# Kernel tuning notes

Hardware: AMD Instinct MI355X
Metric: run time of the kernel (lower is better)

## Reference

```python
import jax, jax.numpy as jnp
import numpy as np

N = 256           # rotation dimension (rows of X)
B = 8192          # columns / batch of vectors being rotated
N_THETAS = N * (N - 1) // 2


def _schedule(n):
    """Round-robin (circle method) tournament schedule.

    Returns pa, pb, tix each of shape [n-1, n//2]:
      round r applies disjoint Givens rotations to row pairs (pa[r,k], pb[r,k])
      using theta index tix[r,k] (lexicographic index of pair (i,j), i<j).
    """
    arr = list(range(n))
    pa, pb, tix = [], [], []
    for _ in range(n - 1):
        ra, rb, rt = [], [], []
        for k in range(n // 2):
            i, j = arr[k], arr[n - 1 - k]
            if i > j:
                i, j = j, i
            ra.append(i)
            rb.append(j)
            rt.append(i * n - i * (i + 1) // 2 + (j - i - 1))
        pa.append(ra)
        pb.append(rb)
        tix.append(rt)
        arr = [arr[0], arr[-1]] + arr[1:-1]
    return np.array(pa), np.array(pb), np.array(tix)


def setup_inputs() -> dict:
    key = jax.random.key(0)
    k1, k2 = jax.random.split(key)
    X = jax.random.normal(k1, (N, B), dtype=jnp.float32)
    thetas = jax.random.normal(k2, (N_THETAS,), dtype=jnp.float32) * 0.1
    return {"X": X, "thetas": thetas}


def reference(X, thetas):
    n = X.shape[0]
    pa_np, pb_np, tix_np = _schedule(n)          # static numpy, traced-time constants
    th = thetas[jnp.asarray(tix_np)]             # [n-1, n//2]
    c, s = jnp.cos(th), jnp.sin(th)
    pa = jnp.asarray(pa_np)
    pb = jnp.asarray(pb_np)

    def step(Xc, inp):
        a, b, cr, sr = inp                        # a,b: [n//2] row indices (disjoint)
        ra, rb = Xc[a], Xc[b]                     # [n//2, B]
        Xc = Xc.at[a].set(cr[:, None] * ra - sr[:, None] * rb)
        Xc = Xc.at[b].set(sr[:, None] * ra + cr[:, None] * rb)
        return Xc, None

    Xo, _ = jax.lax.scan(step, X, (pa, pb, c, s))  # n-1 sequential rounds
    return Xo
```

## Files before the change

kernel.cpp:

```cpp
#include <hip/hip_runtime.h>

#define NROT 256
#define NB   8192
#define TBL_ROUNDS 264

typedef _Float16 f16;
typedef _Float16 f16x8 __attribute__((ext_vector_type(8)));
typedef float    f32x4 __attribute__((ext_vector_type(4)));


__global__ void k_prep(const float* __restrict__ thetas, float4* __restrict__ tbl) {
    int idx = blockIdx.x * 256 + threadIdx.x;
    if (idx >= TBL_ROUNDS * 128) return;
    int r = idx >> 7;
    int k = idx & 127;
    if (r >= 255) {
        tbl[idx] = make_float4(1.0f, 0.0f, __int_as_float(0 | (1 << 16)), 0.0f);
        return;
    }
    int i, j;
    if (k == 0) {
        i = 0;
        j = (254 - r) + 1;
    } else {
        int m1 = k - 1 - r;   if (m1 < 0) m1 += 255;
        int m2 = 254 - k - r; if (m2 < 0) m2 += 255;
        int v1 = m1 + 1, v2 = m2 + 1;
        i = v1 < v2 ? v1 : v2;
        j = v1 < v2 ? v2 : v1;
    }
    int tix = i * 256 - (i * (i + 1)) / 2 + (j - i - 1);
    float th = thetas[tix];
    float s, c;
    sincosf(th, &s, &c);
    tbl[idx] = make_float4(c, s, __int_as_float(i | (j << 16)), 0.0f);
}

template <int ROFF>
__device__ __forceinline__ void rot_rounds64(const float4* __restrict__ t0, float* buf) {
    float4 e0[4], e1[4];
#pragma unroll
    for (int d = 0; d < 4; ++d) {
        e0[d] = t0[(ROFF + d) * 128];
        e1[d] = t0[(ROFF + d) * 128 + 1];
    }
#pragma unroll 4
    for (int it = 0; it < 64; ++it) {
        const int slot = it % 4;
        float4 E0 = e0[slot], E1 = e1[slot];
        e0[slot] = t0[(ROFF + it + 4) * 128];
        e1[slot] = t0[(ROFF + it + 4) * 128 + 1];

        int ij0 = __float_as_int(E0.z);
        int a0 = ij0 & 0xffff, b0 = ij0 >> 16;
        int ij1 = __float_as_int(E1.z);
        int a1 = ij1 & 0xffff, b1 = ij1 >> 16;

        float ra0 = buf[a0], rb0 = buf[b0];
        float ra1 = buf[a1], rb1 = buf[b1];
        float na0 = E0.x * ra0 - E0.y * rb0;
        float nb0 = E0.y * ra0 + E0.x * rb0;
        float na1 = E1.x * ra1 - E1.y * rb1;
        float nb1 = E1.y * ra1 + E1.x * rb1;
        buf[a0] = na0; buf[b0] = nb0;
        buf[a1] = na1; buf[b1] = nb1;
    }
}

__global__ __launch_bounds__(64) void k_rot(const float4* __restrict__ tbl,
                                            float* __restrict__ Rg) {
    __shared__ float buf[256];
    int l   = threadIdx.x;
    int grp = blockIdx.y;
    int c   = blockIdx.x;
#pragma unroll
    for (int q = 0; q < 4; ++q) {
        int m = l * 4 + q;
        buf[m] = (m == c) ? 1.0f : 0.0f;
    }
    const float4* t0 = tbl + 2 * l;
    if      (grp == 0) rot_rounds64<0>(t0, buf);
    else if (grp == 1) rot_rounds64<64>(t0, buf);
    else if (grp == 2) rot_rounds64<128>(t0, buf);
    else               rot_rounds64<192>(t0, buf);

    float* Rout = Rg + grp * (256 * 256);
#pragma unroll
    for (int q = 0; q < 4; ++q) {
        int m = l * 4 + q;
        Rout[m * 256 + c] = buf[m];
    }
}

__global__ __launch_bounds__(256) void k_merge4(const float* __restrict__ Rg,
                                                f16* __restrict__ Rh) {
    __shared__ float vcur[256];
    __shared__ float pacc[4][256];
    int t = threadIdx.x;
    int w = t >> 6;
    int l = t & 63;
    int r0 = blockIdx.x;

    if (t < 64)
        *(float4*)&vcur[t * 4] =
            *(const float4*)(Rg + 3 * 65536 + r0 * 256 + t * 4);
    __syncthreads();

    for (int g = 2; g >= 0; --g) {
        const float* A = Rg + g * 65536;
        int kbase = w * 64;
        float4 acc = make_float4(0.f, 0.f, 0.f, 0.f);
#pragma unroll 8
        for (int kk = 0; kk < 64; ++kk) {
            float  s = vcur[kbase + kk];
            float4 a = *(const float4*)(A + (kbase + kk) * 256 + l * 4);
            acc.x += s * a.x; acc.y += s * a.y;
            acc.z += s * a.z; acc.w += s * a.w;
        }
        *(float4*)&pacc[w][l * 4] = acc;
        __syncthreads();
        if (t < 64) {
            float4 p0 = *(float4*)&pacc[0][t * 4];
            float4 p1 = *(float4*)&pacc[1][t * 4];
            float4 p2 = *(float4*)&pacc[2][t * 4];
            float4 p3 = *(float4*)&pacc[3][t * 4];
            float4 sum = make_float4(p0.x + p1.x + p2.x + p3.x,
                                     p0.y + p1.y + p2.y + p3.y,
                                     p0.z + p1.z + p2.z + p3.z,
                                     p0.w + p1.w + p2.w + p3.w);
            if (g > 0) *(float4*)&vcur[t * 4] = sum;
            else {
                int o = r0 * 256 + t * 4;
                Rh[o + 0] = (f16)sum.x;
                Rh[o + 1] = (f16)sum.y;
                Rh[o + 2] = (f16)sum.z;
                Rh[o + 3] = (f16)sum.w;
            }
        }
        __syncthreads();
    }
}

__global__ __launch_bounds__(512) void k_gemm(const f16* __restrict__ Rh,
                                              const float* __restrict__ X,
                                              float* __restrict__ out) {
    __shared__ float Xf[256][32];
    __shared__ __align__(16) f16 Xh[32 * 256];
    int t  = threadIdx.x;
    int w  = t >> 6;
    int l  = t & 63;
    int n0 = blockIdx.x * 32;

#pragma unroll
    for (int p = 0; p < 4; ++p) {
        int idx = t + 512 * p;
        int n4  = idx & 7;
        int k   = idx >> 3;
        *(float4*)&Xf[k][n4 * 4] =
            *(const float4*)(X + (size_t)k * NB + n0 + n4 * 4);
    }
    __syncthreads();

    {
        int n  = t & 31;
        int k0 = (t >> 5) * 16;
        f16x8 h0, h1;
#pragma unroll
        for (int u = 0; u < 8; ++u) h0[u] = (f16)Xf[k0 + u][n];
#pragma unroll
        for (int u = 0; u < 8; ++u) h1[u] = (f16)Xf[k0 + 8 + u][n];
        int xv = (n & 7) * 8;
        *(f16x8*)&Xh[n * 256 + ((k0    ) ^ xv)] = h0;
        *(f16x8*)&Xh[n * 256 + ((k0 + 8) ^ xv)] = h1;
    }
    __syncthreads();

    f32x4 acc[2][2];
#pragma unroll
    for (int r = 0; r < 2; ++r)
#pragma unroll
        for (int c = 0; c < 2; ++c) acc[r][c] = (f32x4){0.f, 0.f, 0.f, 0.f};

    int lm = l & 15;
    int g  = l >> 4;
    int xv = (lm & 7) * 8;
#pragma unroll
    for (int s = 0; s < 8; ++s) {
        int koff = s * 32 + 8 * g;
        f16x8 a0 = *(const f16x8*)(Rh + (32 * w + lm) * 256 + koff);
        f16x8 a1 = *(const f16x8*)(Rh + (32 * w + 16 + lm) * 256 + koff);
        f16x8 b0 = *(const f16x8*)&Xh[lm * 256        + (koff ^ xv)];
        f16x8 b1 = *(const f16x8*)&Xh[(16 + lm) * 256 + (koff ^ xv)];
        acc[0][0] = __builtin_amdgcn_mfma_f32_16x16x32_f16(a0, b0, acc[0][0], 0, 0, 0);
        acc[0][1] = __builtin_amdgcn_mfma_f32_16x16x32_f16(a0, b1, acc[0][1], 0, 0, 0);
        acc[1][0] = __builtin_amdgcn_mfma_f32_16x16x32_f16(a1, b0, acc[1][0], 0, 0, 0);
        acc[1][1] = __builtin_amdgcn_mfma_f32_16x16x32_f16(a1, b1, acc[1][1], 0, 0, 0);
    }

#pragma unroll
    for (int r = 0; r < 2; ++r)
#pragma unroll
        for (int c = 0; c < 2; ++c)
#pragma unroll
            for (int q = 0; q < 4; ++q)
                out[(size_t)(32 * w + 16 * r + 4 * g + q) * NB + n0 + 16 * c + lm] =
                    acc[r][c][q];
}

extern "C" void kernel_launch(void* const* d_in, const int* in_sizes, int n_in,
                              void* d_out, int out_size, void* d_ws, size_t ws_size,
                              hipStream_t stream) {
    const float* X      = (const float*)d_in[0];
    const float* thetas = (const float*)d_in[1];
    float* out = (float*)d_out;
    char*  ws  = (char*)d_ws;

    float4* tbl = (float4*)ws;
    float*  Rg  = (float*)(ws + 540672);
    f16*    Rh  = (f16*)(ws + 1589248);

    k_prep  <<<dim3(132),    dim3(256), 0, stream>>>(thetas, tbl);
    k_rot   <<<dim3(256, 4), dim3(64),  0, stream>>>(tbl, Rg);
    k_merge4<<<dim3(256),    dim3(256), 0, stream>>>(Rg, Rh);
    k_gemm  <<<dim3(256),    dim3(512), 0, stream>>>(Rh, X, out);
}
```

Before: 39.42 us.

## Keep rotation state in registers with wave shuffles and tree-merge partial products

```diff
diff --git a/kernel.cpp b/kernel.cpp
--- a/kernel.cpp
+++ b/kernel.cpp
@@ -5,140 +5,144 @@
 #define TBL_ROUNDS 264
 
 typedef _Float16 f16;
+typedef _Float16 f16x4 __attribute__((ext_vector_type(4)));
 typedef _Float16 f16x8 __attribute__((ext_vector_type(8)));
 typedef float    f32x4 __attribute__((ext_vector_type(4)));
 
 
-__global__ void k_prep(const float* __restrict__ thetas, float4* __restrict__ tbl) {
+__global__ void k_prep(const float* __restrict__ thetas, float2* __restrict__ cs) {
     int idx = blockIdx.x * 256 + threadIdx.x;
     if (idx >= TBL_ROUNDS * 128) return;
     int r = idx >> 7;
     int k = idx & 127;
-    if (r >= 255) {
-        tbl[idx] = make_float4(1.0f, 0.0f, __int_as_float(0 | (1 << 16)), 0.0f);
-        return;
-    }
+    if (r >= 255) { cs[idx] = make_float2(1.0f, 0.0f); return; }
     int i, j;
+    bool swapped = false;
     if (k == 0) {
         i = 0;
-        j = (254 - r) + 1;
+        j = 255 - r;
     } else {
         int m1 = k - 1 - r;   if (m1 < 0) m1 += 255;
         int m2 = 254 - k - r; if (m2 < 0) m2 += 255;
         int v1 = m1 + 1, v2 = m2 + 1;
-        i = v1 < v2 ? v1 : v2;
-        j = v1 < v2 ? v2 : v1;
+        swapped = v1 > v2;
+        i = swapped ? v2 : v1;
+        j = swapped ? v1 : v2;
     }
     int tix = i * 256 - (i * (i + 1)) / 2 + (j - i - 1);
     float th = thetas[tix];
     float s, c;
     sincosf(th, &s, &c);
-    tbl[idx] = make_float4(c, s, __int_as_float(i | (j << 16)), 0.0f);
-}
-
-template <int ROFF>
-__device__ __forceinline__ void rot_rounds64(const float4* __restrict__ t0, float* buf) {
-    float4 e0[4], e1[4];
-#pragma unroll
-    for (int d = 0; d < 4; ++d) {
-        e0[d] = t0[(ROFF + d) * 128];
-        e1[d] = t0[(ROFF + d) * 128 + 1];
-    }
+    cs[idx] = make_float2(c, swapped ? -s : s);
+}
+
+__device__ __forceinline__ int rowOf(int p, int R) {
+    if (p == 0) return 0;
+    int m = (p - 1 - R) % 255;
+    if (m < 0) m += 255;
+    return m + 1;
+}
+
+__global__ __launch_bounds__(64) void k_rot(const float4* __restrict__ csf4,
+                                            float* __restrict__ Rg) {
+    int l    = threadIdx.x;
+    int grp  = blockIdx.y;
+    int c    = blockIdx.x;
+    int ROFF = grp * 64;
+
+    int pA0 = 2 * l, pA1 = 2 * l + 1, pB1 = 254 - 2 * l, pB0 = 255 - 2 * l;
+
+    float A0 = (rowOf(pA0, ROFF) == c) ? 1.0f : 0.0f;
+    float A1 = (rowOf(pA1, ROFF) == c) ? 1.0f : 0.0f;
+    float B1 = (rowOf(pB1, ROFF) == c) ? 1.0f : 0.0f;
+    float B0 = (rowOf(pB0, ROFF) == c) ? 1.0f : 0.0f;
+
+    float4 ring[4];
+#pragma unroll
+    for (int d = 0; d < 4; ++d) ring[d] = csf4[(ROFF + d) * 64 + l];
+
 #pragma unroll 4
     for (int it = 0; it < 64; ++it) {
-        const int slot = it % 4;
-        float4 E0 = e0[slot], E1 = e1[slot];
-        e0[slot] = t0[(ROFF + it + 4) * 128];
-        e1[slot] = t0[(ROFF + it + 4) * 128 + 1];
-
-        int ij0 = __float_as_int(E0.z);
-        int a0 = ij0 & 0xffff, b0 = ij0 >> 16;
-        int ij1 = __float_as_int(E1.z);
-        int a1 = ij1 & 0xffff, b1 = ij1 >> 16;
-
-        float ra0 = buf[a0], rb0 = buf[b0];
-        float ra1 = buf[a1], rb1 = buf[b1];
-        float na0 = E0.x * ra0 - E0.y * rb0;
-        float nb0 = E0.y * ra0 + E0.x * rb0;
-        float na1 = E1.x * ra1 - E1.y * rb1;
-        float nb1 = E1.y * ra1 + E1.x * rb1;
-        buf[a0] = na0; buf[b0] = nb0;
-        buf[a1] = na1; buf[b1] = nb1;
-    }
-}
-
-__global__ __launch_bounds__(64) void k_rot(const float4* __restrict__ tbl,
-                                            float* __restrict__ Rg) {
-    __shared__ float buf[256];
-    int l   = threadIdx.x;
-    int grp = blockIdx.y;
-    int c   = blockIdx.x;
-#pragma unroll
-    for (int q = 0; q < 4; ++q) {
-        int m = l * 4 + q;
-        buf[m] = (m == c) ? 1.0f : 0.0f;
-    }
-    const float4* t0 = tbl + 2 * l;
-    if      (grp == 0) rot_rounds64<0>(t0, buf);
-    else if (grp == 1) rot_rounds64<64>(t0, buf);
-    else if (grp == 2) rot_rounds64<128>(t0, buf);
-    else               rot_rounds64<192>(t0, buf);
-
+        const int slot = it & 3;
+        float4 CS = ring[slot];
+        ring[slot] = csf4[(ROFF + it + 4) * 64 + l];
+
+        float nA0 = CS.x * A0 - CS.y * B0;
+        float nB0 = CS.y * A0 + CS.x * B0;
+        float nA1 = CS.z * A1 - CS.w * B1;
+        float nB1 = CS.w * A1 + CS.z * B1;
+
+        float upA1 = __shfl_up(nA1, 1);
+        float dnB0 = __shfl_down(nB0, 1);
+
+        A0 = (l == 0)  ? nA0 : upA1;
+        A1 = (l == 0)  ? nB0 : nA0;
+        B0 = nB1;
+        B1 = (l == 63) ? nA1 : dnB0;
+    }
+
+    int R = ROFF + 64;
     float* Rout = Rg + grp * (256 * 256);
-#pragma unroll
-    for (int q = 0; q < 4; ++q) {
-        int m = l * 4 + q;
-        Rout[m * 256 + c] = buf[m];
-    }
-}
-
-__global__ __launch_bounds__(256) void k_merge4(const float* __restrict__ Rg,
-                                                f16* __restrict__ Rh) {
-    __shared__ float vcur[256];
-    __shared__ float pacc[4][256];
-    int t = threadIdx.x;
-    int w = t >> 6;
-    int l = t & 63;
-    int r0 = blockIdx.x;
-
-    if (t < 64)
-        *(float4*)&vcur[t * 4] =
-            *(const float4*)(Rg + 3 * 65536 + r0 * 256 + t * 4);
+    Rout[rowOf(pA0, R) * 256 + c] = A0;
+    Rout[rowOf(pA1, R) * 256 + c] = A1;
+    Rout[rowOf(pB1, R) * 256 + c] = B1;
+    Rout[rowOf(pB0, R) * 256 + c] = B0;
+}
+
+__device__ __forceinline__ void merge_tile(const float* __restrict__ B,
+                                           const float* __restrict__ A,
+                                           float (*Vs)[260], int t,
+                                           int r0, int c0, float4* accp) {
+#pragma unroll
+    for (int p = 0; p < 4; ++p) {
+        int idx = t + 256 * p;
+        int row = idx >> 6;
+        int k4  = (idx & 63) * 4;
+        *(float4*)&Vs[row][k4] = *(const float4*)(B + (r0 + row) * 256 + k4);
+    }
     __syncthreads();
 
-    for (int g = 2; g >= 0; --g) {
-        const float* A = Rg + g * 65536;
-        int kbase = w * 64;
-        float4 acc = make_float4(0.f, 0.f, 0.f, 0.f);
+    int r  = t >> 4;
+    int c4 = (t & 15) * 4;
+    float4 acc = make_float4(0.f, 0.f, 0.f, 0.f);
 #pragma unroll 8
-        for (int kk = 0; kk < 64; ++kk) {
-            float  s = vcur[kbase + kk];
-            float4 a = *(const float4*)(A + (kbase + kk) * 256 + l * 4);
-            acc.x += s * a.x; acc.y += s * a.y;
-            acc.z += s * a.z; acc.w += s * a.w;
-        }
-        *(float4*)&pacc[w][l * 4] = acc;
-        __syncthreads();
-        if (t < 64) {
-            float4 p0 = *(float4*)&pacc[0][t * 4];
-            float4 p1 = *(float4*)&pacc[1][t * 4];
-            float4 p2 = *(float4*)&pacc[2][t * 4];
-            float4 p3 = *(float4*)&pacc[3][t * 4];
-            float4 sum = make_float4(p0.x + p1.x + p2.x + p3.x,
-                                     p0.y + p1.y + p2.y + p3.y,
-                                     p0.z + p1.z + p2.z + p3.z,
-                                     p0.w + p1.w + p2.w + p3.w);
-            if (g > 0) *(float4*)&vcur[t * 4] = sum;
-            else {
-                int o = r0 * 256 + t * 4;
-                Rh[o + 0] = (f16)sum.x;
-                Rh[o + 1] = (f16)sum.y;
-                Rh[o + 2] = (f16)sum.z;
-                Rh[o + 3] = (f16)sum.w;
-            }
-        }
-        __syncthreads();
-    }
+    for (int k = 0; k < 256; ++k) {
+        float  av = Vs[r][k];
+        float4 a  = *(const float4*)(A + k * 256 + c0 + c4);
+        acc.x += av * a.x; acc.y += av * a.y;
+        acc.z += av * a.z; acc.w += av * a.w;
+    }
+    *accp = acc;
+}
+
+__global__ __launch_bounds__(256) void k_mergeL1(const float* __restrict__ Rg,
+                                                 float* __restrict__ Pg) {
+    __shared__ float Vs[16][260];
+    int t  = threadIdx.x;
+    int c0 = blockIdx.x * 64;
+    int r0 = blockIdx.y * 16;
+    int z  = blockIdx.z;
+    const float* A = Rg + (2 * z) * 65536;
+    const float* B = Rg + (2 * z + 1) * 65536;
+    float4 acc;
+    merge_tile(B, A, Vs, t, r0, c0, &acc);
+    int r = t >> 4, c4 = (t & 15) * 4;
+    *(float4*)(Pg + z * 65536 + (r0 + r) * 256 + c0 + c4) = acc;
+}
+
+__global__ __launch_bounds__(256) void k_mergeL2(const float* __restrict__ Pg,
+                                                 f16* __restrict__ Rh) {
+    __shared__ float Vs[16][260];
+    int t  = threadIdx.x;
+    int c0 = blockIdx.x * 64;
+    int r0 = blockIdx.y * 16;
+    const float* A = Pg;
+    const float* B = Pg + 65536;
+    float4 acc;
+    merge_tile(B, A, Vs, t, r0, c0, &acc);
+    int r = t >> 4, c4 = (t & 15) * 4;
+    f16x4 h = { (f16)acc.x, (f16)acc.y, (f16)acc.z, (f16)acc.w };
+    *(f16x4*)(Rh + (r0 + r) * 256 + c0 + c4) = h;
 }
 
 __global__ __launch_bounds__(512) void k_gemm(const f16* __restrict__ Rh,
@@ -215,12 +219,15 @@
     float* out = (float*)d_out;
     char*  ws  = (char*)d_ws;
 
-    float4* tbl = (float4*)ws;
-    float*  Rg  = (float*)(ws + 540672);
-    f16*    Rh  = (f16*)(ws + 1589248);
-
-    k_prep  <<<dim3(132),    dim3(256), 0, stream>>>(thetas, tbl);
-    k_rot   <<<dim3(256, 4), dim3(64),  0, stream>>>(tbl, Rg);
-    k_merge4<<<dim3(256),    dim3(256), 0, stream>>>(Rg, Rh);
-    k_gemm  <<<dim3(256),    dim3(512), 0, stream>>>(Rh, X, out);
-}
+    float2* cs   = (float2*)ws;
+    float4* csf4 = (float4*)ws;
+    float*  Rg   = (float*)(ws + 270336);
+    float*  Pg   = (float*)(ws + 1318912);
+    f16*    Rh   = (f16*)(ws + 1843200);
+
+    k_prep   <<<dim3(132),      dim3(256), 0, stream>>>(thetas, cs);
+    k_rot    <<<dim3(256, 4),   dim3(64),  0, stream>>>(csf4, Rg);
+    k_mergeL1<<<dim3(4, 16, 2), dim3(256), 0, stream>>>(Rg, Pg);
+    k_mergeL2<<<dim3(4, 16),    dim3(256), 0, stream>>>(Pg, Rh);
+    k_gemm   <<<dim3(256),      dim3(512), 0, stream>>>(Rh, X, out);
+}
```

After: 50.21 us. +27.4%, slower.
